# Performance work log

Hardware: AMD Instinct MI355X
Metric: run time of the kernel (lower is better)

Reference implementation:

```python
import jax, jax.numpy as jnp
import numpy as np

B, L, D, H, DK, DV, FF, V, N = 1, 1024, 1024, 16, 64, 64, 4096, 32000, 12


def _ln(x, s, b):
    mu = jnp.mean(x, axis=-1, keepdims=True)
    var = jnp.mean((x - mu) ** 2, axis=-1, keepdims=True)
    return (x - mu) / jnp.sqrt(var + 1e-5) * s + b


def _pe(length, d):
    # interleaved sin/cos positional encoding, matching stack([sin,cos],-1).view(L,D)
    i = 2.0 * jnp.arange(d // 2, dtype=jnp.float32)
    base = 10000.0 ** (-i / d)
    half = jnp.arange(length, dtype=jnp.float32)[:, None] * base[None, :]  # [L, D/2]
    return jnp.stack([jnp.sin(half), jnp.cos(half)], axis=-1).reshape(length, d)


def setup_inputs() -> dict:
    key = jax.random.key(0)
    ks = jax.random.split(key, 8)
    s = 0.02
    return {
        "tokens": jax.random.randint(ks[0], (B, L), 0, V),
        "emb": jax.random.normal(ks[1], (V, D), jnp.float32) * s,
        "final_b": jnp.zeros((V,), jnp.float32),
        "Wq": jax.random.normal(ks[2], (N, H, D, DK), jnp.float32) * s,
        "Wk": jax.random.normal(ks[3], (N, H, D, DK), jnp.float32) * s,
        "Wv": jax.random.normal(ks[4], (N, H, D, DV), jnp.float32) * s,
        "Wo": jax.random.normal(ks[5], (N, H * DV, D), jnp.float32) * s,
        "ln1_s": jnp.ones((N, D), jnp.float32),
        "ln1_b": jnp.zeros((N, D), jnp.float32),
        "W1": jax.random.normal(ks[6], (N, D, FF), jnp.float32) * s,
        "b1": jnp.zeros((N, FF), jnp.float32),
        "W2": jax.random.normal(ks[7], (N, FF, D), jnp.float32) * s,
        "b2": jnp.zeros((N, D), jnp.float32),
        "ln2_s": jnp.ones((N, D), jnp.float32),
        "ln2_b": jnp.zeros((N, D), jnp.float32),
    }


def _forward(tokens, emb, final_b, Wq, Wk, Wv, Wo, ln1_s, ln1_b, W1, b1, W2, b2, ln2_s, ln2_b):
    a = emb[tokens] * jnp.sqrt(jnp.float32(3.0 * D))  # tied-weight scaling
    a = a + (a + _pe(L, D))  # faithful to `a += pe(a)` where pe returns x + PE
    mask = jnp.tril(jnp.ones((L, L), dtype=bool))
    scale = 1.0 / jnp.sqrt(jnp.float32(D))  # original divides by sqrt(d_model), not d_k

    def layer(x, p):
        wq, wk, wv, wo, s1, sb1, w1, bb1, w2, bb2, s2, sb2 = p
        q = jnp.einsum('bld,hdk->bhlk', x, wq)
        k = jnp.einsum('bld,hdk->bhlk', x, wk)
        v = jnp.einsum('bld,hdv->bhlv', x, wv)
        scores = jnp.einsum('bhqk,bhmk->bhqm', q, k) * scale  # [B,H,L,L]
        scores = jnp.where(mask, scores, -jnp.inf)  # causal triu(-inf)
        attn = jax.nn.softmax(scores, axis=-1)
        o = jnp.einsum('bhqm,bhmv->bhqv', attn, v)
        o = o.transpose(0, 2, 1, 3).reshape(x.shape[0], L, H * DV)  # concat heads
        x = _ln(x + o @ wo, s1, sb1)  # post-LN residual
        f = jax.nn.relu(x @ w1 + bb1) @ w2 + bb2
        x = _ln(x + f, s2, sb2)
        return x, None

    x, _ = jax.lax.scan(layer, a, (Wq, Wk, Wv, Wo, ln1_s, ln1_b, W1, b1, W2, b2, ln2_s, ln2_b))
    return x @ emb.T + final_b  # tied output projection with bias


def reference(tokens, emb, final_b, Wq, Wk, Wv, Wo, ln1_s, ln1_b, W1, b1, W2, b2, ln2_s, ln2_b):
    return _forward(tokens, emb, final_b, Wq, Wk, Wv, Wo, ln1_s, ln1_b, W1, b1, W2, b2, ln2_s, ln2_b)
```

## Files before the change

kernel.cpp:

```cpp
#include <hip/hip_runtime.h>

typedef unsigned short u16;
typedef __attribute__((ext_vector_type(8))) short short8;
typedef __attribute__((ext_vector_type(4))) float f32x4;
typedef __attribute__((ext_vector_type(4))) u16 u16x4;

#define LSEQ   1024
#define DMODEL 1024
#define NHEAD  16
#define DHEAD  64
#define DFF    4096
#define NLAYER 12
#define NVOCAB 32000

__device__ __forceinline__ u16 f2b(float f) {
  union { float f; unsigned u; } x; x.f = f;
  unsigned r = x.u + 0x7fffu + ((x.u >> 16) & 1u);
  return (u16)(r >> 16);
}

__device__ __forceinline__ f32x4 mfma16(short8 a, short8 b, f32x4 c) {
  return __builtin_amdgcn_mfma_f32_16x16x32_bf16(a, b, c, 0, 0, 0);
}

__device__ __forceinline__ void gload16(const u16* g, u16* l) {
  __builtin_amdgcn_global_load_lds(
      (const __attribute__((address_space(1))) void*)g,
      (__attribute__((address_space(3))) void*)l, 16, 0, 0);
}

__global__ __launch_bounds__(256) void embed_k(const int* __restrict__ tok,
    const float* __restrict__ emb, float* __restrict__ x, u16* __restrict__ xb)
{
  const int l = blockIdx.x;
  const int d0 = threadIdx.x * 4;
  const int t = tok[l];
  const float lf = (float)l;
  float o[4]; u16 obv[4];
#pragma unroll
  for (int j = 0; j < 4; ++j) {
    int d = d0 + j;
    int p = d >> 1;
    float ang = lf * powf(10000.0f, -(float)(2 * p) / 1024.0f);
    float pe = (d & 1) ? cosf(ang) : sinf(ang);
    float val = 2.0f * emb[(size_t)t * DMODEL + d] * 55.42562584220407f + pe;
    o[j] = val; obv[j] = f2b(val);
  }
  *reinterpret_cast<float4*>(x + (size_t)l * DMODEL + d0) = make_float4(o[0], o[1], o[2], o[3]);
  u16x4 vb = { obv[0], obv[1], obv[2], obv[3] };
  *reinterpret_cast<u16x4*>(xb + (size_t)l * DMODEL + d0) = vb;
}

__global__ __launch_bounds__(256) void ln_k(const float* __restrict__ xin,
    const float* __restrict__ yin, const float* __restrict__ s, const float* __restrict__ b,
    float* __restrict__ xout, u16* __restrict__ xbout)
{
  const int row = blockIdx.x, tid = threadIdx.x;
  const int d0 = tid * 4;
  float4 xv = *reinterpret_cast<const float4*>(xin + (size_t)row * DMODEL + d0);
  float4 yv = *reinterpret_cast<const float4*>(yin + (size_t)row * DMODEL + d0);
  float t0 = xv.x + yv.x, t1 = xv.y + yv.y, t2 = xv.z + yv.z, t3 = xv.w + yv.w;
  float sum = t0 + t1 + t2 + t3;
  float sq  = t0 * t0 + t1 * t1 + t2 * t2 + t3 * t3;
#pragma unroll
  for (int d = 1; d < 64; d <<= 1) { sum += __shfl_xor(sum, d); sq += __shfl_xor(sq, d); }
  __shared__ float ssum[4], ssq[4];
  const int wid = tid >> 6;
  if ((tid & 63) == 0) { ssum[wid] = sum; ssq[wid] = sq; }
  __syncthreads();
  sum = ssum[0] + ssum[1] + ssum[2] + ssum[3];
  sq  = ssq[0] + ssq[1] + ssq[2] + ssq[3];
  const float mu = sum * (1.0f / 1024.0f);
  const float var = sq * (1.0f / 1024.0f) - mu * mu;
  const float rstd = rsqrtf(var + 1e-5f);
  float4 sv = *reinterpret_cast<const float4*>(s + d0);
  float4 bv = *reinterpret_cast<const float4*>(b + d0);
  float o0 = (t0 - mu) * rstd * sv.x + bv.x;
  float o1 = (t1 - mu) * rstd * sv.y + bv.y;
  float o2 = (t2 - mu) * rstd * sv.z + bv.z;
  float o3 = (t3 - mu) * rstd * sv.w + bv.w;
  *reinterpret_cast<float4*>(xout + (size_t)row * DMODEL + d0) = make_float4(o0, o1, o2, o3);
  u16x4 vb = { f2b(o0), f2b(o1), f2b(o2), f2b(o3) };
  *reinterpret_cast<u16x4*>(xbout + (size_t)row * DMODEL + d0) = vb;
}

__global__ __launch_bounds__(256) void tconv_k(const float* __restrict__ in, u16* __restrict__ out,
                                               int R, int C, int zper, int lstride, int obase, int zstride)
{
  __shared__ float t[64][65];
  const int rt = blockIdx.y * 64, ct = blockIdx.x * 64;
  const int z = blockIdx.z;
  in += (size_t)z * zstride;
  const int tr = threadIdx.x >> 4, tc = threadIdx.x & 15;
#pragma unroll
  for (int i = 0; i < 4; ++i) {
    int r = i * 16 + tr;
    float4 v = *reinterpret_cast<const float4*>(in + (size_t)(rt + r) * C + ct + tc * 4);
    t[r][tc * 4 + 0] = v.x; t[r][tc * 4 + 1] = v.y;
    t[r][tc * 4 + 2] = v.z; t[r][tc * 4 + 3] = v.w;
  }
  __syncthreads();
  const size_t orow0 = (size_t)(z / zper) * lstride + (size_t)(z % zper) * C + obase + ct;
#pragma unroll
  for (int i = 0; i < 4; ++i) {
    int c = i * 16 + tr;
    u16x4 o;
    o[0] = f2b(t[tc * 4 + 0][c]); o[1] = f2b(t[tc * 4 + 1][c]);
    o[2] = f2b(t[tc * 4 + 2][c]); o[3] = f2b(t[tc * 4 + 3][c]);
    *reinterpret_cast<u16x4*>(out + (orow0 + c) * R + rt + tc * 4) = o;
  }
}

__global__ __launch_bounds__(256) void ec_k(const float* __restrict__ in, u16* __restrict__ out)
{
  const size_t i = ((size_t)blockIdx.x * 256 + threadIdx.x) * 8;
  float4 a = *reinterpret_cast<const float4*>(in + i);
  float4 b = *reinterpret_cast<const float4*>(in + i + 4);
  short8 o;
  o[0] = f2b(a.x); o[1] = f2b(a.y); o[2] = f2b(a.z); o[3] = f2b(a.w);
  o[4] = f2b(b.x); o[5] = f2b(b.y); o[6] = f2b(b.z); o[7] = f2b(b.w);
  *reinterpret_cast<short8*>(out + i) = o;
}

template<int BM, int BN, int BK, int BSRC, bool BIAS, bool RELU, int OUTMODE>
__global__ __launch_bounds__(256) void gemm_bt(
    const u16* __restrict__ A, int lda,
    const void* __restrict__ Bp, int ldb,
    const float* __restrict__ bias,
    void* __restrict__ Cv, int ldc, int Ktot)
{
  const int tid = threadIdx.x, lane = tid & 63, wid = tid >> 6;
  const int nwg = gridDim.x * gridDim.y;
  const int flat = blockIdx.y * gridDim.x + blockIdx.x;
  const int qq = nwg >> 3;
  const int ni = (flat & 7) * qq + (flat >> 3);
  const int m0 = (ni % gridDim.x) * BM, n0 = (ni / gridDim.x) * BN;
  constexpr int FM = BM / 32, FN = BN / 32;
  constexpr int KS = BK / 32;
  constexpr int CPR = BK / 8;
  constexpr int SWM = CPR - 1;
  const int wm = (wid >> 1) * (BM / 2), wn = (wid & 1) * (BN / 2);
  f32x4 acc[FM][FN] = {};

  if constexpr (BSRC == 0) {
    __shared__ u16 As[2][BM * BK];
    __shared__ u16 Bs[2][BN * BK];
    const u16* Bt = (const u16*)Bp;

    auto stage = [&](int buf, int k0) {
#pragma unroll
      for (int i = 0; i < (BM * CPR) / 256; ++i) {
        int c = i * 256 + wid * 64 + lane;
        int row = c / CPR, p0 = c % CPR;
        int part = p0 ^ (row & SWM);
        gload16(A + (size_t)(m0 + row) * lda + k0 + part * 8,
                &As[buf][(i * 256 + wid * 64) * 8]);
      }
#pragma unroll
      for (int i = 0; i < (BN * CPR) / 256; ++i) {
        int c = i * 256 + wid * 64 + lane;
        int row = c / CPR, p0 = c % CPR;
        int part = p0 ^ (row & SWM);
        gload16(Bt + (size_t)(n0 + row) * ldb + k0 + part * 8,
                &Bs[buf][(i * 256 + wid * 64) * 8]);
      }
    };

    stage(0, 0);
    asm volatile("s_waitcnt vmcnt(0)" ::: "memory");
    __builtin_amdgcn_s_barrier();
    asm volatile("" ::: "memory");

    const int NT = Ktot / BK;
    int cur = 0;
    for (int t = 0; t < NT; ++t) {
      if (t + 1 < NT) stage(cur ^ 1, (t + 1) * BK);
      asm volatile("" ::: "memory");
      short8 a[KS][FM], b[KS][FN];
#pragma unroll
      for (int ks = 0; ks < KS; ++ks) {
#pragma unroll
        for (int fm = 0; fm < FM; ++fm) {
          int row = wm + fm * 16 + (lane & 15);
          int pidx = (ks * 4 + (lane >> 4)) ^ (row & SWM);
          a[ks][fm] = *reinterpret_cast<const short8*>(&As[cur][row * BK + pidx * 8]);
        }
#pragma unroll
        for (int fn = 0; fn < FN; ++fn) {
          int row = wn + fn * 16 + (lane & 15);
          int pidx = (ks * 4 + (lane >> 4)) ^ (row & SWM);
          b[ks][fn] = *reinterpret_cast<const short8*>(&Bs[cur][row * BK + pidx * 8]);
        }
      }
#pragma unroll
      for (int ks = 0; ks < KS; ++ks)
#pragma unroll
        for (int fm = 0; fm < FM; ++fm)
#pragma unroll
          for (int fn = 0; fn < FN; ++fn)
            acc[fm][fn] = mfma16(a[ks][fm], b[ks][fn], acc[fm][fn]);
      asm volatile("s_waitcnt vmcnt(0)" ::: "memory");
      __builtin_amdgcn_s_barrier();
      asm volatile("" ::: "memory");
      cur ^= 1;
    }
  } else {
    __shared__ u16 As[BM * BK];
    __shared__ u16 Bs[BN * BK];
    const float* Bf = (const float*)Bp;
    for (int k0 = 0; k0 < Ktot; k0 += BK) {
#pragma unroll
      for (int i = 0; i < (BM * CPR) / 256; ++i) {
        int c = i * 256 + wid * 64 + lane;
        int row = c / CPR, part = c % CPR;
        gload16(A + (size_t)(m0 + row) * lda + k0 + part * 8,
                &As[(i * 256 + wid * 64) * 8]);
      }
      {
        int row = tid >> 1, kh = (tid & 1) * 16;
        const float* src = Bf + (size_t)(n0 + row) * ldb + k0 + kh;
        float4 v0 = *reinterpret_cast<const float4*>(src);
        float4 v1 = *reinterpret_cast<const float4*>(src + 4);
        float4 v2 = *reinterpret_cast<const float4*>(src + 8);
        float4 v3 = *reinterpret_cast<const float4*>(src + 12);
        short8 p0, p1;
        p0[0] = f2b(v0.x); p0[1] = f2b(v0.y); p0[2] = f2b(v0.z); p0[3] = f2b(v0.w);
        p0[4] = f2b(v1.x); p0[5] = f2b(v1.y); p0[6] = f2b(v1.z); p0[7] = f2b(v1.w);
        p1[0] = f2b(v2.x); p1[1] = f2b(v2.y); p1[2] = f2b(v2.z); p1[3] = f2b(v2.w);
        p1[4] = f2b(v3.x); p1[5] = f2b(v3.y); p1[6] = f2b(v3.z); p1[7] = f2b(v3.w);
        *reinterpret_cast<short8*>(&Bs[row * BK + kh])     = p0;
        *reinterpret_cast<short8*>(&Bs[row * BK + kh + 8]) = p1;
      }
      __syncthreads();
      short8 a[KS][FM], b[KS][FN];
#pragma unroll
      for (int ks = 0; ks < KS; ++ks) {
#pragma unroll
        for (int fm = 0; fm < FM; ++fm) {
          int row = wm + fm * 16 + (lane & 15);
          a[ks][fm] = *reinterpret_cast<const short8*>(&As[row * BK + (ks * 4 + (lane >> 4)) * 8]);
        }
#pragma unroll
        for (int fn = 0; fn < FN; ++fn) {
          int row = wn + fn * 16 + (lane & 15);
          b[ks][fn] = *reinterpret_cast<const short8*>(&Bs[row * BK + (ks * 4 + (lane >> 4)) * 8]);
        }
      }
#pragma unroll
      for (int ks = 0; ks < KS; ++ks)
#pragma unroll
        for (int fm = 0; fm < FM; ++fm)
#pragma unroll
          for (int fn = 0; fn < FN; ++fn)
            acc[fm][fn] = mfma16(a[ks][fm], b[ks][fn], acc[fm][fn]);
      __syncthreads();
    }
  }

#pragma unroll
  for (int fm = 0; fm < FM; ++fm) {
#pragma unroll
    for (int fn = 0; fn < FN; ++fn) {
#pragma unroll
      for (int r = 0; r < 4; ++r) {
        int row = m0 + wm + fm * 16 + (lane >> 4) * 4 + r;
        int col = n0 + wn + fn * 16 + (lane & 15);
        float val = acc[fm][fn][r];
        if (BIAS) val += bias[col];
        if (RELU) val = fmaxf(val, 0.0f);
        if (OUTMODE == 0) {
          ((float*)Cv)[(size_t)row * ldc + col] = val;
        } else if (OUTMODE == 1) {
          ((u16*)Cv)[(size_t)row * ldc + col] = f2b(val);
        } else {
          int sel = col >> 10, cc = col & 1023;
          ((u16*)Cv)[(size_t)sel * (LSEQ * DMODEL) + (size_t)row * DMODEL + cc] = f2b(val);
        }
      }
    }
  }
}

__global__ __launch_bounds__(256) void attn_k(const u16* __restrict__ q,
    const u16* __restrict__ kmat, const u16* __restrict__ v, u16* __restrict__ o)
{
  __shared__ u16 Ks[64][72];
  __shared__ u16 Vt[64][72];
  __shared__ u16 Pl[4][16][72];
  const int tid = threadIdx.x, lane = tid & 63, wid = tid >> 6;
  const int h = blockIdx.y, qt = blockIdx.x;
  const int qw0 = qt * 64 + wid * 16;
  const int qrow = qw0 + (lane & 15);
  const short8 aq0 = *reinterpret_cast<const short8*>(q + (size_t)qrow * DMODEL + h * DHEAD + (lane >> 4) * 8);
  const short8 aq1 = *reinterpret_cast<const short8*>(q + (size_t)qrow * DMODEL + h * DHEAD + 32 + (lane >> 4) * 8);
  float m_run[4], l_run[4];
  f32x4 oacc[4] = {};
#pragma unroll
  for (int r = 0; r < 4; ++r) { m_run[r] = -1e30f; l_run[r] = 0.0f; }
  const int kvend = qt * 64 + 64;

  for (int kv0 = 0; kv0 < kvend; kv0 += 64) {
    {
      int kvi = tid >> 2, c16 = (tid & 3) * 16;
      const u16* kp = kmat + (size_t)(kv0 + kvi) * DMODEL + h * DHEAD + c16;
      *reinterpret_cast<short8*>(&Ks[kvi][c16])     = *reinterpret_cast<const short8*>(kp);
      *reinterpret_cast<short8*>(&Ks[kvi][c16 + 8]) = *reinterpret_cast<const short8*>(kp + 8);
      const u16* vp = v + (size_t)(kv0 + kvi) * DMODEL + h * DHEAD + c16;
      short8 v0 = *reinterpret_cast<const short8*>(vp);
      short8 v1 = *reinterpret_cast<const short8*>(vp + 8);
#pragma unroll
      for (int j = 0; j < 8; ++j) { Vt[c16 + j][kvi] = (u16)v0[j]; Vt[c16 + 8 + j][kvi] = (u16)v1[j]; }
    }
    __syncthreads();

    float sm[4][4];
#pragma unroll
    for (int t2 = 0; t2 < 4; ++t2) {
      short8 bk0 = *reinterpret_cast<const short8*>(&Ks[t2 * 16 + (lane & 15)][(lane >> 4) * 8]);
      short8 bk1 = *reinterpret_cast<const short8*>(&Ks[t2 * 16 + (lane & 15)][32 + (lane >> 4) * 8]);
      f32x4 s4 = {};
      s4 = mfma16(aq0, bk0, s4);
      s4 = mfma16(aq1, bk1, s4);
#pragma unroll
      for (int r = 0; r < 4; ++r) {
        int rowg = qw0 + (lane >> 4) * 4 + r;
        int colg = kv0 + t2 * 16 + (lane & 15);
        float val = s4[r] * 0.03125f;
        sm[t2][r] = (colg <= rowg) ? val : -1e30f;
      }
    }
    float alpha[4], p[4][4];
#pragma unroll
    for (int r = 0; r < 4; ++r) {
      float mx = fmaxf(fmaxf(sm[0][r], sm[1][r]), fmaxf(sm[2][r], sm[3][r]));
#pragma unroll
      for (int d = 1; d < 16; d <<= 1) mx = fmaxf(mx, __shfl_xor(mx, d));
      float mn = fmaxf(m_run[r], mx);
      alpha[r] = __expf(m_run[r] - mn);
      float ps = 0.0f;
#pragma unroll
      for (int t2 = 0; t2 < 4; ++t2) { p[t2][r] = __expf(sm[t2][r] - mn); ps += p[t2][r]; }
#pragma unroll
      for (int d = 1; d < 16; d <<= 1) ps += __shfl_xor(ps, d);
      l_run[r] = l_run[r] * alpha[r] + ps;
      m_run[r] = mn;
    }
#pragma unroll
    for (int fn = 0; fn < 4; ++fn) {
      f32x4 t = oacc[fn];
      t[0] *= alpha[0]; t[1] *= alpha[1]; t[2] *= alpha[2]; t[3] *= alpha[3];
      oacc[fn] = t;
    }
#pragma unroll
    for (int r = 0; r < 4; ++r) {
      int rit = (lane >> 4) * 4 + r;
#pragma unroll
      for (int t2 = 0; t2 < 4; ++t2)
        Pl[wid][rit][t2 * 16 + (lane & 15)] = f2b(p[t2][r]);
    }
    short8 pa0 = *reinterpret_cast<const short8*>(&Pl[wid][lane & 15][(lane >> 4) * 8]);
    short8 pa1 = *reinterpret_cast<const short8*>(&Pl[wid][lane & 15][32 + (lane >> 4) * 8]);
#pragma unroll
    for (int fn = 0; fn < 4; ++fn) {
      short8 bv0 = *reinterpret_cast<const short8*>(&Vt[fn * 16 + (lane & 15)][(lane >> 4) * 8]);
      short8 bv1 = *reinterpret_cast<const short8*>(&Vt[fn * 16 + (lane & 15)][32 + (lane >> 4) * 8]);
      oacc[fn] = mfma16(pa0, bv0, oacc[fn]);
      oacc[fn] = mfma16(pa1, bv1, oacc[fn]);
    }
    __syncthreads();
  }
#pragma unroll
  for (int fn = 0; fn < 4; ++fn) {
#pragma unroll
    for (int r = 0; r < 4; ++r) {
      int row = qw0 + (lane >> 4) * 4 + r;
      float val = oacc[fn][r] / l_run[r];
      o[(size_t)row * DMODEL + h * DHEAD + fn * 16 + (lane & 15)] = f2b(val);
    }
  }
}

extern "C" void kernel_launch(void* const* d_in, const int* in_sizes, int n_in,
                              void* d_out, int out_size, void* d_ws, size_t ws_size,
                              hipStream_t stream) {
  (void)in_sizes; (void)n_in; (void)out_size;
  const int*   tok    = (const int*)d_in[0];
  const float* emb    = (const float*)d_in[1];
  const float* finalb = (const float*)d_in[2];
  const float* Wq     = (const float*)d_in[3];
  const float* Wk     = (const float*)d_in[4];
  const float* Wv     = (const float*)d_in[5];
  const float* Wo     = (const float*)d_in[6];
  const float* ln1s   = (const float*)d_in[7];
  const float* ln1b   = (const float*)d_in[8];
  const float* W1     = (const float*)d_in[9];
  const float* b1     = (const float*)d_in[10];
  const float* W2     = (const float*)d_in[11];
  const float* b2     = (const float*)d_in[12];
  const float* ln2s   = (const float*)d_in[13];
  const float* ln2b   = (const float*)d_in[14];
  float* out = (float*)d_out;

  float* x   = (float*)d_ws;
  float* y   = x + LSEQ * DMODEL;
  u16* xb    = (u16*)(y + LSEQ * DMODEL);
  u16* qb    = xb + LSEQ * DMODEL;
  u16* kb    = qb + LSEQ * DMODEL;
  u16* vb    = kb + LSEQ * DMODEL;
  u16* ob    = vb + LSEQ * DMODEL;
  u16* h1    = ob + LSEQ * DMODEL;
  u16* wbase = h1 + LSEQ * DFF;

  const size_t eQKV = (size_t)3 * DMODEL * DMODEL;
  const size_t eWO  = (size_t)DMODEL * DMODEL;
  const size_t eW1  = (size_t)DFF * DMODEL;
  const size_t eW2  = (size_t)DMODEL * DFF;
  const size_t perL = eQKV + eWO + eW1 + eW2;
  const size_t eEMB = (size_t)NVOCAB * DMODEL;
  const size_t actE = (size_t)(wbase - (u16*)d_ws);
  const size_t bigNeed = (actE + NLAYER * perL + eEMB) * 2;
  const size_t midNeed = (actE + perL + eEMB) * 2;
  const int mode = ws_size >= bigNeed ? 2 : (ws_size >= midNeed ? 1 : 0);
  const int WL = (mode == 2) ? NLAYER : 1;

  u16* qkvT = wbase;
  u16* woT  = qkvT + WL * eQKV;
  u16* w1T  = woT  + WL * eWO;
  u16* w2T  = w1T  + WL * eW1;
  u16* embT = w2T  + WL * eW2;

  if (mode == 2) {
    tconv_k<<<dim3(1, 16, 192), 256, 0, stream>>>(Wq, qkvT, DMODEL, DHEAD, 16, 3 * DMODEL, 0,    DMODEL * DHEAD);
    tconv_k<<<dim3(1, 16, 192), 256, 0, stream>>>(Wk, qkvT, DMODEL, DHEAD, 16, 3 * DMODEL, 1024, DMODEL * DHEAD);
    tconv_k<<<dim3(1, 16, 192), 256, 0, stream>>>(Wv, qkvT, DMODEL, DHEAD, 16, 3 * DMODEL, 2048, DMODEL * DHEAD);
    tconv_k<<<dim3(16, 16, 12), 256, 0, stream>>>(Wo, woT, DMODEL, DMODEL, 1, DMODEL, 0, DMODEL * DMODEL);
    tconv_k<<<dim3(64, 16, 12), 256, 0, stream>>>(W1, w1T, DMODEL, DFF, 1, DFF, 0, DMODEL * DFF);
    tconv_k<<<dim3(16, 64, 12), 256, 0, stream>>>(W2, w2T, DFF, DMODEL, 1, DMODEL, 0, DFF * DMODEL);
    ec_k<<<(NVOCAB * DMODEL) / 2048, 256, 0, stream>>>(emb, embT);
  } else if (mode == 1) {
    ec_k<<<(NVOCAB * DMODEL) / 2048, 256, 0, stream>>>(emb, embT);
  }

  embed_k<<<LSEQ, 256, 0, stream>>>(tok, emb, x, xb);

  for (int l = 0; l < NLAYER; ++l) {
    const float* wq  = Wq + (size_t)l * NHEAD * DMODEL * DHEAD;
    const float* wk  = Wk + (size_t)l * NHEAD * DMODEL * DHEAD;
    const float* wv  = Wv + (size_t)l * NHEAD * DMODEL * DHEAD;
    const float* wo  = Wo + (size_t)l * DMODEL * DMODEL;
    const float* w1  = W1 + (size_t)l * DMODEL * DFF;
    const float* b1l = b1 + (size_t)l * DFF;
    const float* w2  = W2 + (size_t)l * DFF * DMODEL;
    const float* b2l = b2 + (size_t)l * DMODEL;
    u16* qkvTl = qkvT + (mode == 2 ? (size_t)l * eQKV : 0);
    u16* woTl  = woT  + (mode == 2 ? (size_t)l * eWO  : 0);
    u16* w1Tl  = w1T  + (mode == 2 ? (size_t)l * eW1  : 0);
    u16* w2Tl  = w2T  + (mode == 2 ? (size_t)l * eW2  : 0);

    if (mode < 2) {
      tconv_k<<<dim3(1, 16, 16), 256, 0, stream>>>(wq, qkvTl, DMODEL, DHEAD, 16, 0, 0,    DMODEL * DHEAD);
      tconv_k<<<dim3(1, 16, 16), 256, 0, stream>>>(wk, qkvTl, DMODEL, DHEAD, 16, 0, 1024, DMODEL * DHEAD);
      tconv_k<<<dim3(1, 16, 16), 256, 0, stream>>>(wv, qkvTl, DMODEL, DHEAD, 16, 0, 2048, DMODEL * DHEAD);
      tconv_k<<<dim3(16, 16, 1), 256, 0, stream>>>(wo, woTl, DMODEL, DMODEL, 1, 0, 0, 0);
      tconv_k<<<dim3(64, 16, 1), 256, 0, stream>>>(w1, w1Tl, DMODEL, DFF, 1, 0, 0, 0);
      tconv_k<<<dim3(16, 64, 1), 256, 0, stream>>>(w2, w2Tl, DFF, DMODEL, 1, 0, 0, 0);
    }

    gemm_bt<64, 128, 64, 0, false, false, 2><<<dim3(16, 24), 256, 0, stream>>>(
        xb, DMODEL, qkvTl, DMODEL, nullptr, qb, DMODEL, DMODEL);
    attn_k<<<dim3(16, 16), 256, 0, stream>>>(qb, kb, vb, ob);
    gemm_bt<64, 64, 64, 0, false, false, 0><<<dim3(16, 16), 256, 0, stream>>>(
        ob, DMODEL, woTl, DMODEL, nullptr, y, DMODEL, DMODEL);
    ln_k<<<LSEQ, 256, 0, stream>>>(x, y, ln1s + (size_t)l * DMODEL, ln1b + (size_t)l * DMODEL, x, xb);
    gemm_bt<64, 128, 64, 0, true, true, 1><<<dim3(16, 32), 256, 0, stream>>>(
        xb, DMODEL, w1Tl, DMODEL, b1l, h1, DFF, DMODEL);
    gemm_bt<64, 64, 64, 0, true, false, 0><<<dim3(16, 16), 256, 0, stream>>>(
        h1, DFF, w2Tl, DFF, b2l, y, DMODEL, DFF);
    ln_k<<<LSEQ, 256, 0, stream>>>(x, y, ln2s + (size_t)l * DMODEL, ln2b + (size_t)l * DMODEL, x, xb);
  }

  if (mode >= 1) {
    gemm_bt<128, 128, 64, 0, true, false, 0><<<dim3(8, 250), 256, 0, stream>>>(
        xb, DMODEL, embT, DMODEL, finalb, out, NVOCAB, DMODEL);
  } else {
    gemm_bt<128, 128, 32, 1, true, false, 0><<<dim3(8, 250), 256, 0, stream>>>(
        xb, DMODEL, emb, DMODEL, finalb, out, NVOCAB, DMODEL);
  }
}
```

Before: 2.114 ms.

## Split-K output and FF2 GEMMs with reduction fused into LayerNorm, enlarge tiles

Measured after the change: 1.950 ms. 7.7% less time.

```diff
diff --git a/kernel.cpp b/kernel.cpp
--- a/kernel.cpp
+++ b/kernel.cpp
@@ -52,14 +52,23 @@
 }
 
 __global__ __launch_bounds__(256) void ln_k(const float* __restrict__ xin,
-    const float* __restrict__ yin, const float* __restrict__ s, const float* __restrict__ b,
+    const float* __restrict__ ypart, int P, const float* __restrict__ ybias,
+    const float* __restrict__ s, const float* __restrict__ b,
     float* __restrict__ xout, u16* __restrict__ xbout)
 {
   const int row = blockIdx.x, tid = threadIdx.x;
   const int d0 = tid * 4;
   float4 xv = *reinterpret_cast<const float4*>(xin + (size_t)row * DMODEL + d0);
-  float4 yv = *reinterpret_cast<const float4*>(yin + (size_t)row * DMODEL + d0);
-  float t0 = xv.x + yv.x, t1 = xv.y + yv.y, t2 = xv.z + yv.z, t3 = xv.w + yv.w;
+  float t0 = xv.x, t1 = xv.y, t2 = xv.z, t3 = xv.w;
+#pragma unroll 2
+  for (int p = 0; p < P; ++p) {
+    float4 yv = *reinterpret_cast<const float4*>(ypart + (size_t)p * (LSEQ * DMODEL) + (size_t)row * DMODEL + d0);
+    t0 += yv.x; t1 += yv.y; t2 += yv.z; t3 += yv.w;
+  }
+  if (ybias) {
+    float4 bb = *reinterpret_cast<const float4*>(ybias + d0);
+    t0 += bb.x; t1 += bb.y; t2 += bb.z; t3 += bb.w;
+  }
   float sum = t0 + t1 + t2 + t3;
   float sq  = t0 * t0 + t1 * t1 + t2 * t2 + t3 * t3;
 #pragma unroll
@@ -122,7 +131,7 @@
   *reinterpret_cast<short8*>(out + i) = o;
 }
 
-template<int BM, int BN, int BK, int BSRC, bool BIAS, bool RELU, int OUTMODE>
+template<int BM, int BN, int BK, int BSRC, bool BIAS, bool RELU, int OUTMODE, int KSPLIT>
 __global__ __launch_bounds__(256) void gemm_bt(
     const u16* __restrict__ A, int lda,
     const void* __restrict__ Bp, int ldb,
@@ -135,6 +144,8 @@
   const int qq = nwg >> 3;
   const int ni = (flat & 7) * qq + (flat >> 3);
   const int m0 = (ni % gridDim.x) * BM, n0 = (ni / gridDim.x) * BN;
+  const int kbase = (KSPLIT > 1) ? blockIdx.z * (Ktot / KSPLIT) : 0;
+  const int klen  = (KSPLIT > 1) ? (Ktot / KSPLIT) : Ktot;
   constexpr int FM = BM / 32, FN = BN / 32;
   constexpr int KS = BK / 32;
   constexpr int CPR = BK / 8;
@@ -166,15 +177,15 @@
       }
     };
 
-    stage(0, 0);
+    stage(0, kbase);
     asm volatile("s_waitcnt vmcnt(0)" ::: "memory");
     __builtin_amdgcn_s_barrier();
     asm volatile("" ::: "memory");
 
-    const int NT = Ktot / BK;
+    const int NT = klen / BK;
     int cur = 0;
     for (int t = 0; t < NT; ++t) {
-      if (t + 1 < NT) stage(cur ^ 1, (t + 1) * BK);
+      if (t + 1 < NT) stage(cur ^ 1, kbase + (t + 1) * BK);
       asm volatile("" ::: "memory");
       short8 a[KS][FM], b[KS][FN];
 #pragma unroll
@@ -257,6 +268,7 @@
     }
   }
 
+  const size_t pbase = (KSPLIT > 1) ? (size_t)blockIdx.z * gridDim.x * BM * ldc : 0;
 #pragma unroll
   for (int fm = 0; fm < FM; ++fm) {
 #pragma unroll
@@ -269,7 +281,7 @@
         if (BIAS) val += bias[col];
         if (RELU) val = fmaxf(val, 0.0f);
         if (OUTMODE == 0) {
-          ((float*)Cv)[(size_t)row * ldc + col] = val;
+          ((float*)Cv)[pbase + (size_t)row * ldc + col] = val;
         } else if (OUTMODE == 1) {
           ((u16*)Cv)[(size_t)row * ldc + col] = f2b(val);
         } else {
@@ -410,6 +422,8 @@
   u16* ob    = vb + LSEQ * DMODEL;
   u16* h1    = ob + LSEQ * DMODEL;
   u16* wbase = h1 + LSEQ * DFF;
+  float* woPart  = (float*)h1;
+  float* ff2Part = (float*)qb;
 
   const size_t eQKV = (size_t)3 * DMODEL * DMODEL;
   const size_t eWO  = (size_t)DMODEL * DMODEL;
@@ -466,24 +480,26 @@
       tconv_k<<<dim3(16, 64, 1), 256, 0, stream>>>(w2, w2Tl, DFF, DMODEL, 1, 0, 0, 0);
     }
 
-    gemm_bt<64, 128, 64, 0, false, false, 2><<<dim3(16, 24), 256, 0, stream>>>(
+    gemm_bt<128, 128, 64, 0, false, false, 2, 1><<<dim3(8, 24), 256, 0, stream>>>(
         xb, DMODEL, qkvTl, DMODEL, nullptr, qb, DMODEL, DMODEL);
     attn_k<<<dim3(16, 16), 256, 0, stream>>>(qb, kb, vb, ob);
-    gemm_bt<64, 64, 64, 0, false, false, 0><<<dim3(16, 16), 256, 0, stream>>>(
-        ob, DMODEL, woTl, DMODEL, nullptr, y, DMODEL, DMODEL);
-    ln_k<<<LSEQ, 256, 0, stream>>>(x, y, ln1s + (size_t)l * DMODEL, ln1b + (size_t)l * DMODEL, x, xb);
-    gemm_bt<64, 128, 64, 0, true, true, 1><<<dim3(16, 32), 256, 0, stream>>>(
+    gemm_bt<128, 64, 64, 0, false, false, 0, 2><<<dim3(8, 16, 2), 256, 0, stream>>>(
+        ob, DMODEL, woTl, DMODEL, nullptr, woPart, DMODEL, DMODEL);
+    ln_k<<<LSEQ, 256, 0, stream>>>(x, woPart, 2, nullptr,
+        ln1s + (size_t)l * DMODEL, ln1b + (size_t)l * DMODEL, x, xb);
+    gemm_bt<128, 128, 64, 0, true, true, 1, 1><<<dim3(8, 32), 256, 0, stream>>>(
         xb, DMODEL, w1Tl, DMODEL, b1l, h1, DFF, DMODEL);
-    gemm_bt<64, 64, 64, 0, true, false, 0><<<dim3(16, 16), 256, 0, stream>>>(
-        h1, DFF, w2Tl, DFF, b2l, y, DMODEL, DFF);
-    ln_k<<<LSEQ, 256, 0, stream>>>(x, y, ln2s + (size_t)l * DMODEL, ln2b + (size_t)l * DMODEL, x, xb);
+    gemm_bt<128, 64, 64, 0, false, false, 0, 2><<<dim3(8, 16, 2), 256, 0, stream>>>(
+        h1, DFF, w2Tl, DFF, nullptr, ff2Part, DMODEL, DFF);
+    ln_k<<<LSEQ, 256, 0, stream>>>(x, ff2Part, 2, b2l,
+        ln2s + (size_t)l * DMODEL, ln2b + (size_t)l * DMODEL, x, xb);
   }
 
   if (mode >= 1) {
-    gemm_bt<128, 128, 64, 0, true, false, 0><<<dim3(8, 250), 256, 0, stream>>>(
+    gemm_bt<128, 128, 64, 0, true, false, 0, 1><<<dim3(8, 250), 256, 0, stream>>>(
         xb, DMODEL, embT, DMODEL, finalb, out, NVOCAB, DMODEL);
   } else {
-    gemm_bt<128, 128, 32, 1, true, false, 0><<<dim3(8, 250), 256, 0, stream>>>(
+    gemm_bt<128, 128, 32, 1, true, false, 0, 1><<<dim3(8, 250), 256, 0, stream>>>(
         xb, DMODEL, emb, DMODEL, finalb, out, NVOCAB, DMODEL);
   }
 }
```
